# Kernel tuning notes

Measured on AMD Instinct MI355X. Metric: run time of the kernel, lower is better.

## Reference

```python
import jax, jax.numpy as jnp
import numpy as np

N = 50000
E = 400000
F_IN = 5
H = 8
C1, C2, C3 = 64, 32, 16
NEG_SLOPE = 0.2


def setup_inputs() -> dict:
    key = jax.random.key(0)
    ks = jax.random.split(key, 16)
    s = 0.1  # small init scale
    return {
        "x": jax.random.normal(ks[0], (N, F_IN), jnp.float32),
        "edge_index": jax.random.randint(ks[1], (2, E), 0, N, jnp.int64),
        "edge_weight": jax.random.uniform(ks[2], (E,), jnp.float32),
        "W1": jax.random.normal(ks[3], (F_IN, H * C1), jnp.float32) * s,
        "a_src1": jax.random.normal(ks[4], (H, C1), jnp.float32) * s,
        "a_dst1": jax.random.normal(ks[5], (H, C1), jnp.float32) * s,
        "b1": jnp.zeros((H * C1,), jnp.float32),
        "W2": jax.random.normal(ks[6], (H * C1, H * C2), jnp.float32) * s,
        "a_src2": jax.random.normal(ks[7], (H, C2), jnp.float32) * s,
        "a_dst2": jax.random.normal(ks[8], (H, C2), jnp.float32) * s,
        "b2": jnp.zeros((H * C2,), jnp.float32),
        "Wg": jax.random.normal(ks[9], (H * C2, C3), jnp.float32) * s,
        "bg": jnp.zeros((C3,), jnp.float32),
        "Wfc": jax.random.normal(ks[10], (C3, 1), jnp.float32) * s,
        "bfc": jnp.zeros((1,), jnp.float32),
    }


def _gat_layer(x, W, a_src, a_dst, b, src, dst, n, heads, ch):
    # PyG GATConv (concat=True), eval mode (dropout off), self-loops already in src/dst.
    h = (x @ W).reshape(n, heads, ch)                      # (N, H, C)
    e_s = jnp.sum(h * a_src, axis=-1)                      # (N, H)
    e_d = jnp.sum(h * a_dst, axis=-1)                      # (N, H)
    e = jax.nn.leaky_relu(e_s[src] + e_d[dst], NEG_SLOPE)  # (Etot, H)
    m = jax.ops.segment_max(e, dst, num_segments=n)
    m = jnp.where(jnp.isfinite(m), m, 0.0)                 # guard empty segments
    ex = jnp.exp(e - m[dst])
    den = jax.ops.segment_sum(ex, dst, num_segments=n)
    alpha = ex / (den[dst] + 1e-16)                        # softmax over in-edges
    out = jax.ops.segment_sum(h[src] * alpha[..., None], dst, num_segments=n)
    return out.reshape(n, heads * ch) + b


def _gcn_layer(x, W, b, src, dst, w_full, n):
    # PyG GCNConv with gcn_norm: D^{-1/2} A_hat D^{-1/2}, self-loop weight 1.
    deg = jax.ops.segment_sum(w_full, dst, num_segments=n)
    dinv = jnp.where(deg > 0, jax.lax.rsqrt(deg), 0.0)
    norm = dinv[src] * w_full * dinv[dst]                  # (Etot,)
    h = x @ W                                              # (N, C3)
    out = jax.ops.segment_sum(h[src] * norm[:, None], dst, num_segments=n)
    return out + b


def reference(x, edge_index, edge_weight, W1, a_src1, a_dst1, b1,
              W2, a_src2, a_dst2, b2, Wg, bg, Wfc, bfc):
    n = x.shape[0]
    loops = jnp.arange(n, dtype=edge_index.dtype)
    src = jnp.concatenate([edge_index[0], loops])
    dst = jnp.concatenate([edge_index[1], loops])
    w_full = jnp.concatenate([edge_weight, jnp.ones((n,), edge_weight.dtype)])

    h = _gat_layer(x, W1, a_src1, a_dst1, b1, src, dst, n, H, C1)
    h = jax.nn.elu(h)
    h = _gat_layer(h, W2, a_src2, a_dst2, b2, src, dst, n, H, C2)
    h = jax.nn.elu(h)
    h = _gcn_layer(h, Wg, bg, src, dst, w_full, n)
    h = jax.nn.elu(h)
    out = jax.nn.sigmoid(h @ Wfc + bfc)                    # (N, 1)
    return out
```

## Files before the change

### kernel.cpp

```cpp
#include <hip/hip_runtime.h>
#include <hip/hip_bf16.h>
#include <float.h>
#include <math.h>

#define N_NODES 50000
#define N_EDGES 400000
#define ETOT    (N_EDGES + N_NODES)
#define F_IN    5
#define HEADS   8
#define C1      64
#define C2      32
#define C3      16
#define HC1     (HEADS * C1)
#define HC2     (HEADS * C2)
#define NEG_SLOPE 0.2f
#define NCHUNK  ((N_NODES + 255) / 256)
#define NH8     (N_NODES * HEADS)
#define MPAD    (((N_NODES + 63) / 64) * 64)
#define GCOLS   (HC2 + 16)
#define PACKBLK ((GCOLS * HC1) / 256)
#define SCATBLK ((ETOT + 255) / 256)
#define ES1BLK  ((NH8 + 255) / 256)

typedef short bf16x8 __attribute__((ext_vector_type(8)));
typedef float f32x4  __attribute__((ext_vector_type(4)));
typedef unsigned short ushort_t;
typedef unsigned short ushort8_t __attribute__((ext_vector_type(8)));

__device__ __forceinline__ float eluf(float x) {
    return x > 0.f ? x : (expf(x) - 1.f);
}
__device__ __forceinline__ float bf2f(unsigned short u) {
    union { unsigned int i; float f; } v; v.i = ((unsigned int)u) << 16; return v.f;
}
__device__ __forceinline__ unsigned short f2bf(float f) {
    __hip_bfloat16 b = __float2bfloat16(f);
    return *(unsigned short*)&b;
}
__device__ __forceinline__ float softnum(float es, float ed) {
    float v = es + ed;
    v = v > 0.f ? v : NEG_SLOPE * v;
    return expf(v);
}

__global__ void k_deg(const int* __restrict__ ei, const float* __restrict__ ew,
                      int* degi, float* degf) {
    int i = blockIdx.x * blockDim.x + threadIdx.x;
    if (i >= ETOT) return;
    int d   = (i < N_EDGES) ? ei[N_EDGES + i] : (i - N_EDGES);
    float w = (i < N_EDGES) ? ew[i] : 1.f;
    atomicAdd(&degi[d], 1);
    atomicAdd(&degf[d], w);
}

__global__ void k_scan_a(const int* __restrict__ deg, int* __restrict__ part) {
    __shared__ int lds[256];
    int t = threadIdx.x;
    int i = blockIdx.x * 256 + t;
    lds[t] = (i < N_NODES) ? deg[i] : 0;
    __syncthreads();
    for (int off = 128; off >= 1; off >>= 1) {
        if (t < off) lds[t] += lds[t + off];
        __syncthreads();
    }
    if (t == 0) part[blockIdx.x] = lds[0];
}

__global__ void k_scan_b(int* part) {
    __shared__ int lds[256];
    int t = threadIdx.x;
    int v = (t < NCHUNK) ? part[t] : 0;
    lds[t] = v;
    __syncthreads();
    for (int off = 1; off < 256; off <<= 1) {
        int x = (t >= off) ? lds[t - off] : 0;
        __syncthreads();
        lds[t] += x;
        __syncthreads();
    }
    if (t < NCHUNK) part[t] = lds[t] - v;
}

__global__ void k_scan_c(const int* __restrict__ deg, const int* __restrict__ part,
                         int* __restrict__ offs) {
    __shared__ int lds[256];
    int t = threadIdx.x;
    int i = blockIdx.x * 256 + t;
    int v = (i < N_NODES) ? deg[i] : 0;
    lds[t] = v;
    __syncthreads();
    for (int off = 1; off < 256; off <<= 1) {
        int x = (t >= off) ? lds[t - off] : 0;
        __syncthreads();
        lds[t] += x;
        __syncthreads();
    }
    int excl = part[blockIdx.x] + lds[t] - v;
    if (i < N_NODES) offs[i] = excl;
    if (i == N_NODES - 1) offs[N_NODES] = excl + v;
}

__global__ void k_prep(const float* __restrict__ W2,
                       const float* __restrict__ a_src2, const float* __restrict__ a_dst2,
                       ushort_t* __restrict__ W2X,
                       const float* __restrict__ W1,
                       const float* __restrict__ a_src1, const float* __restrict__ a_dst1,
                       float* __restrict__ as1f, float* __restrict__ ad1f) {
    if (blockIdx.x < PACKBLK) {
        int idx = blockIdx.x * 256 + threadIdx.x;
        int c = idx >> 9;
        int k = idx & 511;
        float v;
        if (c < HC2) {
            v = W2[(size_t)k * HC2 + c];
        } else {
            int h = (c - HC2) & 7;
            const float* av = (c < HC2 + 8) ? a_src2 : a_dst2;
            v = 0.f;
#pragma unroll 8
            for (int j = 0; j < C2; j++)
                v += W2[(size_t)k * HC2 + h * C2 + j] * av[h * C2 + j];
        }
        W2X[idx] = f2bf(v);
    } else {
        int idx = threadIdx.x;
        if (idx >= HEADS * F_IN) return;
        int h = idx / F_IN, f = idx % F_IN;
        float s = 0.f, d = 0.f;
        for (int c = 0; c < C1; c++) {
            float w = W1[f * HC1 + h * C1 + c];
            s += w * a_src1[h * C1 + c];
            d += w * a_dst1[h * C1 + c];
        }
        as1f[idx] = s;
        ad1f[idx] = d;
    }
}

__global__ void k_scatter_es1(const int* __restrict__ ei, const int* __restrict__ offs,
                              int* cursor, int2* __restrict__ csr,
                              const float* __restrict__ x,
                              const float* __restrict__ as1f, const float* __restrict__ ad1f,
                              float* __restrict__ es, float* __restrict__ ed) {
    if (blockIdx.x < SCATBLK) {
        int i = blockIdx.x * 256 + threadIdx.x;
        if (i >= ETOT) return;
        int s, d;
        if (i < N_EDGES) { s = ei[i]; d = ei[N_EDGES + i]; }
        else             { s = d = i - N_EDGES; }
        int pos = offs[d] + atomicAdd(&cursor[d], 1);
        csr[pos] = make_int2(s, i);
    } else {
        int g = (blockIdx.x - SCATBLK) * 256 + threadIdx.x;
        if (g >= NH8) return;
        int n = g >> 3, h = g & 7;
        float vs = 0.f, vd = 0.f;
#pragma unroll
        for (int f = 0; f < F_IN; f++) {
            float xv = x[n * F_IN + f];
            vs += xv * as1f[h * F_IN + f];
            vd += xv * ad1f[h * F_IN + f];
        }
        es[g] = vs;
        ed[g] = vd;
    }
}

__global__ void k_agg_x(const float* __restrict__ x,
                        const float* __restrict__ es1, const float* __restrict__ ed1,
                        const int* __restrict__ offs, const int2* __restrict__ csr,
                        float* __restrict__ aggx) {
    int g = blockIdx.x * blockDim.x + threadIdx.x;
    if (g >= NH8) return;
    int d = g >> 3, h = g & 7;
    float edv = ed1[g];
    int k0 = offs[d], k1 = offs[d + 1];
    float a0 = 0.f, a1 = 0.f, a2 = 0.f, a3 = 0.f, a4 = 0.f, exsum = 0.f;
    int k = k0;
    if (k + 1 < k1) {
        int2 c0 = csr[k], c1 = csr[k + 1];
        for (; k + 3 < k1; k += 2) {
            int2 n0 = csr[k + 2], n1 = csr[k + 3];
            float x0 = softnum(es1[c0.x * HEADS + h], edv);
            float x1 = softnum(es1[c1.x * HEADS + h], edv);
            const float* xp0 = x + c0.x * F_IN;
            const float* xp1 = x + c1.x * F_IN;
            a0 += x0 * xp0[0] + x1 * xp1[0];
            a1 += x0 * xp0[1] + x1 * xp1[1];
            a2 += x0 * xp0[2] + x1 * xp1[2];
            a3 += x0 * xp0[3] + x1 * xp1[3];
            a4 += x0 * xp0[4] + x1 * xp1[4];
            exsum += x0 + x1;
            c0 = n0; c1 = n1;
        }
        {
            float x0 = softnum(es1[c0.x * HEADS + h], edv);
            float x1 = softnum(es1[c1.x * HEADS + h], edv);
            const float* xp0 = x + c0.x * F_IN;
            const float* xp1 = x + c1.x * F_IN;
            a0 += x0 * xp0[0] + x1 * xp1[0];
            a1 += x0 * xp0[1] + x1 * xp1[1];
            a2 += x0 * xp0[2] + x1 * xp1[2];
            a3 += x0 * xp0[3] + x1 * xp1[3];
            a4 += x0 * xp0[4] + x1 * xp1[4];
            exsum += x0 + x1;
            k += 2;
        }
    }
    if (k < k1) {
        int2 c0 = csr[k];
        float x0 = softnum(es1[c0.x * HEADS + h], edv);
        const float* xp0 = x + c0.x * F_IN;
        a0 += x0 * xp0[0];
        a1 += x0 * xp0[1];
        a2 += x0 * xp0[2];
        a3 += x0 * xp0[3];
        a4 += x0 * xp0[4];
        exsum += x0;
    }
    float inv = 1.f / (exsum + 1e-16f);
    aggx[0 * NH8 + g] = a0 * inv;
    aggx[1 * NH8 + g] = a1 * inv;
    aggx[2 * NH8 + g] = a2 * inv;
    aggx[3 * NH8 + g] = a3 * inv;
    aggx[4 * NH8 + g] = a4 * inv;
}

__global__ __launch_bounds__(256) void k_expand(const float* __restrict__ aggx,
                                                const float* __restrict__ W1,
                                                const float* __restrict__ b1,
                                                ushort_t* __restrict__ x2bf) {
    int wave = threadIdx.x >> 6;
    int j    = threadIdx.x & 63;
    int n    = blockIdx.x * 4 + wave;
    if (n >= N_NODES) return;
    int h = j >> 3;
    int g = n * HEADS + h;
    float av[F_IN];
#pragma unroll
    for (int f = 0; f < F_IN; f++) av[f] = aggx[f * NH8 + g];

    const float* w1p = W1 + j * 8;
    float4 s0 = *(const float4*)(b1 + j * 8);
    float4 s1 = *(const float4*)(b1 + j * 8 + 4);
#pragma unroll
    for (int f = 0; f < F_IN; f++) {
        float4 w0  = *(const float4*)(w1p + f * HC1);
        float4 w1v = *(const float4*)(w1p + f * HC1 + 4);
        s0.x += av[f] * w0.x;  s0.y += av[f] * w0.y;
        s0.z += av[f] * w0.z;  s0.w += av[f] * w0.w;
        s1.x += av[f] * w1v.x; s1.y += av[f] * w1v.y;
        s1.z += av[f] * w1v.z; s1.w += av[f] * w1v.w;
    }
    ushort8_t o;
    o[0] = f2bf(eluf(s0.x)); o[1] = f2bf(eluf(s0.y));
    o[2] = f2bf(eluf(s0.z)); o[3] = f2bf(eluf(s0.w));
    o[4] = f2bf(eluf(s1.x)); o[5] = f2bf(eluf(s1.y));
    o[6] = f2bf(eluf(s1.z)); o[7] = f2bf(eluf(s1.w));
    *(ushort8_t*)(x2bf + (size_t)n * HC1 + j * 8) = o;
}

__global__ __launch_bounds__(256, 3) void k_gemm_mfma(const short* __restrict__ A,
                                                      const short* __restrict__ W2X,
                                                      ushort_t* __restrict__ h2bf,
                                                      float* __restrict__ es2,
                                                      float* __restrict__ ed2) {
    __shared__ short Bs[GCOLS * 32];
    int t    = threadIdx.x;
    int wave = t >> 6;
    int lane = t & 63;
    int lo   = lane & 15;
    int quad = lane >> 4;
    int m0   = blockIdx.x * 64 + wave * 16;
    const short* ap = A + (size_t)(m0 + lo) * HC1 + quad * 8;

    f32x4 acc[17];
#pragma unroll
    for (int f = 0; f < 17; f++) acc[f] = (f32x4){0.f, 0.f, 0.f, 0.f};

    for (int idx = t; idx < GCOLS * 4; idx += 256) {
        int c = idx >> 2, q = idx & 3;
        int s = (q + c + (c >> 2)) & 3;
        *(bf16x8*)(Bs + c * 32 + s * 8) = *(const bf16x8*)(W2X + (size_t)c * HC1 + q * 8);
    }
    __syncthreads();

#pragma unroll 1
    for (int k0 = 0; k0 < HC1; k0 += 32) {
        int nk = k0 + 32;
        bf16x8 pre[5];
        if (nk < HC1) {
#pragma unroll
            for (int j = 0; j < 5; j++) {
                int idx = t + j * 256;
                if (idx < GCOLS * 4) {
                    int c = idx >> 2, q = idx & 3;
                    pre[j] = *(const bf16x8*)(W2X + (size_t)c * HC1 + nk + q * 8);
                }
            }
        }
        bf16x8 aF = *(const bf16x8*)(ap + k0);
#pragma unroll
        for (int f = 0; f < 17; f++) {
            int c = f * 16 + lo;
            int s = (quad + c + (c >> 2)) & 3;
            bf16x8 bF = *(const bf16x8*)(Bs + c * 32 + s * 8);
            acc[f] = __builtin_amdgcn_mfma_f32_16x16x32_bf16(aF, bF, acc[f], 0, 0, 0);
        }
        __syncthreads();
        if (nk < HC1) {
#pragma unroll
            for (int j = 0; j < 5; j++) {
                int idx = t + j * 256;
                if (idx < GCOLS * 4) {
                    int c = idx >> 2, q = idx & 3;
                    int s = (q + c + (c >> 2)) & 3;
                    *(bf16x8*)(Bs + c * 32 + s * 8) = pre[j];
                }
            }
            __syncthreads();
        }
    }

    int rowb = m0 + quad * 4;
#pragma unroll
    for (int f = 0; f < 16; f++) {
#pragma unroll
        for (int r = 0; r < 4; r++) {
            int row = rowb + r;
            if (row < N_NODES)
                h2bf[(size_t)row * HC2 + f * 16 + lo] = f2bf(acc[f][r]);
        }
    }
#pragma unroll
    for (int r = 0; r < 4; r++) {
        int row = rowb + r;
        if (row < N_NODES) {
            if (lo < 8) es2[row * HEADS + lo]       = acc[16][r];
            else        ed2[row * HEADS + (lo - 8)] = acc[16][r];
        }
    }
}

__global__ __launch_bounds__(256) void k_gat_agg2(const ushort_t* __restrict__ h2bf,
                                                  const float* __restrict__ es2,
                                                  const float* __restrict__ ed2,
                                                  const int* __restrict__ offs,
                                                  const int2* __restrict__ csr,
                                                  const float* __restrict__ b2,
                                                  ushort_t* __restrict__ x3bf) {
    int wave = threadIdx.x >> 6;
    int lane = threadIdx.x & 63;
    int d = blockIdx.x * 4 + wave;
    if (d >= N_NODES) return;
    int c4 = lane * 4;
    int h  = lane >> 3;
    float edv = ed2[d * HEADS + h];
    int k0 = offs[d], k1 = offs[d + 1];
    float acc0 = 0.f, acc1 = 0.f, acc2 = 0.f, acc3 = 0.f, exsum = 0.f;
    int k = k0;
    if (k + 1 < k1) {
        int2 e0 = csr[k], e1 = csr[k + 1];
        for (; k + 3 < k1; k += 2) {
            int2 n0 = csr[k + 2], n1 = csr[k + 3];
            float x0 = softnum(es2[e0.x * HEADS + h], edv);
            float x1 = softnum(es2[e1.x * HEADS + h], edv);
            ushort4 v0 = *(const ushort4*)(h2bf + (size_t)e0.x * HC2 + c4);
            ushort4 v1 = *(const ushort4*)(h2bf + (size_t)e1.x * HC2 + c4);
            acc0 += x0 * bf2f(v0.x) + x1 * bf2f(v1.x);
            acc1 += x0 * bf2f(v0.y) + x1 * bf2f(v1.y);
            acc2 += x0 * bf2f(v0.z) + x1 * bf2f(v1.z);
            acc3 += x0 * bf2f(v0.w) + x1 * bf2f(v1.w);
            exsum += x0 + x1;
            e0 = n0; e1 = n1;
        }
        {
            float x0 = softnum(es2[e0.x * HEADS + h], edv);
            float x1 = softnum(es2[e1.x * HEADS + h], edv);
            ushort4 v0 = *(const ushort4*)(h2bf + (size_t)e0.x * HC2 + c4);
            ushort4 v1 = *(const ushort4*)(h2bf + (size_t)e1.x * HC2 + c4);
            acc0 += x0 * bf2f(v0.x) + x1 * bf2f(v1.x);
            acc1 += x0 * bf2f(v0.y) + x1 * bf2f(v1.y);
            acc2 += x0 * bf2f(v0.z) + x1 * bf2f(v1.z);
            acc3 += x0 * bf2f(v0.w) + x1 * bf2f(v1.w);
            exsum += x0 + x1;
            k += 2;
        }
    }
    if (k < k1) {
        int2 e0 = csr[k];
        float x0 = softnum(es2[e0.x * HEADS + h], edv);
        ushort4 v0 = *(const ushort4*)(h2bf + (size_t)e0.x * HC2 + c4);
        acc0 += x0 * bf2f(v0.x);
        acc1 += x0 * bf2f(v0.y);
        acc2 += x0 * bf2f(v0.z);
        acc3 += x0 * bf2f(v0.w);
        exsum += x0;
    }
    float inv = 1.f / (exsum + 1e-16f);
    float4 bias = *(const float4*)(b2 + c4);
    ushort4 o;
    o.x = f2bf(eluf(acc0 * inv + bias.x));
    o.y = f2bf(eluf(acc1 * inv + bias.y));
    o.z = f2bf(eluf(acc2 * inv + bias.z));
    o.w = f2bf(eluf(acc3 * inv + bias.w));
    *(ushort4*)(x3bf + (size_t)d * HC2 + c4) = o;
}

__global__ __launch_bounds__(256) void k_hg(const ushort_t* __restrict__ x3bf,
                                            const float* __restrict__ Wg,
                                            float* __restrict__ hg) {
    __shared__ float xs[16 * HC2];
    int n0 = blockIdx.x * 16;
    int t  = threadIdx.x;
    for (int q = t; q < 16 * HC2 / 4; q += 256) {
        int r  = q >> 6;
        int cc = (q & 63) * 4;
        int n  = n0 + r;
        ushort4 v = make_ushort4(0, 0, 0, 0);
        if (n < N_NODES) v = *(const ushort4*)(x3bf + (size_t)n * HC2 + cc);
        xs[r * HC2 + cc + 0] = bf2f(v.x);
        xs[r * HC2 + cc + 1] = bf2f(v.y);
        xs[r * HC2 + cc + 2] = bf2f(v.z);
        xs[r * HC2 + cc + 3] = bf2f(v.w);
    }
    __syncthreads();
    int r = t >> 4, c = t & 15;
    float acc = 0.f;
#pragma unroll 4
    for (int k = 0; k < HC2; k++) acc += xs[r * HC2 + k] * Wg[k * C3 + c];
    int n = n0 + r;
    if (n < N_NODES) hg[(size_t)n * C3 + c] = acc;
}

__global__ __launch_bounds__(256) void k_gcn_out(const float* __restrict__ hg,
                                                 const float* __restrict__ ew,
                                                 const float* __restrict__ degf,
                                                 const int* __restrict__ offs,
                                                 const int2* __restrict__ csr,
                                                 const float* __restrict__ bg,
                                                 const float* __restrict__ Wfc,
                                                 const float* __restrict__ bfc,
                                                 float* __restrict__ out) {
    int t = threadIdx.x;
    int r = t >> 4, c = t & 15;
    int d = blockIdx.x * 16 + r;
    float val = 0.f;
    if (d < N_NODES) {
        float dd = degf[d];
        float dinv_d = dd > 0.f ? rsqrtf(dd) : 0.f;
        int k0 = offs[d], k1 = offs[d + 1];
        float acc = 0.f;
        for (int k = k0; k < k1; k++) {
            int2 se = csr[k];
            float w = (se.y < N_EDGES) ? ew[se.y] : 1.f;
            float ds_ = degf[se.x];
            float dinv_s = ds_ > 0.f ? rsqrtf(ds_) : 0.f;
            acc += hg[(size_t)se.x * C3 + c] * (dinv_s * w * dinv_d);
        }
        val = eluf(acc + bg[c]);
    }
    float z = val * Wfc[c];
#pragma unroll
    for (int off = 8; off >= 1; off >>= 1) z += __shfl_xor(z, off, 16);
    if (c == 0 && d < N_NODES) out[d] = 1.f / (1.f + expf(-(z + bfc[0])));
}

extern "C" void kernel_launch(void* const* d_in, const int* in_sizes, int n_in,
                              void* d_out, int out_size, void* d_ws, size_t ws_size,
                              hipStream_t stream) {
    const float* x       = (const float*)d_in[0];
    const int*   ei      = (const int*)  d_in[1];
    const float* ew      = (const float*)d_in[2];
    const float* W1      = (const float*)d_in[3];
    const float* a_src1  = (const float*)d_in[4];
    const float* a_dst1  = (const float*)d_in[5];
    const float* b1      = (const float*)d_in[6];
    const float* W2      = (const float*)d_in[7];
    const float* a_src2  = (const float*)d_in[8];
    const float* a_dst2  = (const float*)d_in[9];
    const float* b2      = (const float*)d_in[10];
    const float* Wg      = (const float*)d_in[11];
    const float* bg      = (const float*)d_in[12];
    const float* Wfc     = (const float*)d_in[13];
    const float* bfc     = (const float*)d_in[14];
    float* out = (float*)d_out;

    char* w = (char*)d_ws;
    size_t off = 0;
    auto alloc = [&](size_t bytes) -> void* {
        void* p = w + off;
        off = (off + bytes + 255) & ~(size_t)255;
        return p;
    };
    ushort_t* x2bf = (ushort_t*)alloc((size_t)MPAD * HC1 * 2);
    ushort_t* W2X  = (ushort_t*)alloc((size_t)GCOLS * HC1 * 2);
    ushort_t* h2bf = (ushort_t*)alloc((size_t)N_NODES * HC2 * 2);
    ushort_t* x3bf = (ushort_t*)alloc((size_t)N_NODES * HC2 * 2);
    float* hg     = (float*)alloc((size_t)N_NODES * C3 * 4);
    float* aggx   = (float*)alloc((size_t)F_IN * NH8 * 4);
    float* es1    = (float*)alloc((size_t)NH8 * 4);
    float* ed1    = (float*)alloc((size_t)NH8 * 4);
    float* es2    = (float*)alloc((size_t)NH8 * 4);
    float* ed2    = (float*)alloc((size_t)NH8 * 4);
    float* as1f   = (float*)alloc((size_t)HEADS * F_IN * 4);
    float* ad1f   = (float*)alloc((size_t)HEADS * F_IN * 4);
    float* degf   = (float*)alloc((size_t)N_NODES * 4);
    int*   degi   = (int*)  alloc((size_t)N_NODES * 4);
    int*   cursor = (int*)  alloc((size_t)N_NODES * 4);
    char*  zero_end = w + off;
    int*   offs   = (int*)  alloc((size_t)(N_NODES + 1) * 4);
    int*   part   = (int*)  alloc(256 * 4);
    int2*  csr    = (int2*) alloc((size_t)ETOT * 8);

    const int T = 256;
    hipMemsetAsync(degf, 0, (size_t)(zero_end - (char*)degf), stream);
    k_deg<<<dim3((ETOT + T - 1) / T), dim3(T), 0, stream>>>(ei, ew, degi, degf);
    k_scan_a<<<dim3(NCHUNK), dim3(256), 0, stream>>>(degi, part);
    k_scan_b<<<dim3(1), dim3(256), 0, stream>>>(part);
    k_scan_c<<<dim3(NCHUNK), dim3(256), 0, stream>>>(degi, part, offs);
    k_prep<<<dim3(PACKBLK + 1), dim3(256), 0, stream>>>(
        W2, a_src2, a_dst2, W2X, W1, a_src1, a_dst1, as1f, ad1f);
    k_scatter_es1<<<dim3(SCATBLK + ES1BLK), dim3(256), 0, stream>>>(
        ei, offs, cursor, csr, x, as1f, ad1f, es1, ed1);

    k_agg_x<<<dim3((NH8 + T - 1) / T), dim3(T), 0, stream>>>(x, es1, ed1, offs, csr, aggx);
    k_expand<<<dim3((N_NODES + 3) / 4), dim3(256), 0, stream>>>(aggx, W1, b1, x2bf);

    k_gemm_mfma<<<dim3(MPAD / 64), dim3(256), 0, stream>>>(
        (const short*)x2bf, (const short*)W2X, h2bf, es2, ed2);
    k_gat_agg2<<<dim3((N_NODES + 3) / 4), dim3(256), 0, stream>>>(
        h2bf, es2, ed2, offs, csr, b2, x3bf);

    k_hg<<<dim3((N_NODES + 15) / 16), dim3(256), 0, stream>>>(x3bf, Wg, hg);
    k_gcn_out<<<dim3((N_NODES + 15) / 16), dim3(256), 0, stream>>>(
        hg, ew, degf, offs, csr, bg, Wfc, bfc, out);
}
```

Baseline: 328.3 us.

## Precompute GCN edge norms into CSR, pad x to 8 floats, vectorize hg

The second field of each CSR entry now holds the GCN normalization (dinv[s]*w*dinv[d]) instead of the original edge id. dinv is computed once per node in the scan kernel. This removes the edge-weight and degree gathers and rsqrt work from k_gcn_out, whose loop is also software-pipelined. x is padded to 8 floats per node so the layer-1 aggregation can use float4 loads, and k_hg reads a padded LDS row with float4. The cost is an extra padded copy of x and dinv gathers in the scatter kernel.

```diff
diff --git a/kernel.cpp b/kernel.cpp
--- a/kernel.cpp
+++ b/kernel.cpp
@@ -21,6 +21,8 @@
 #define PACKBLK ((GCOLS * HC1) / 256)
 #define SCATBLK ((ETOT + 255) / 256)
 #define ES1BLK  ((NH8 + 255) / 256)
+#define DEGBLK  SCATBLK
+#define XPBLK   ((N_NODES * 8 + 255) / 256)
 
 typedef short bf16x8 __attribute__((ext_vector_type(8)));
 typedef float f32x4  __attribute__((ext_vector_type(4)));
@@ -44,13 +46,21 @@
 }
 
 __global__ void k_deg(const int* __restrict__ ei, const float* __restrict__ ew,
-                      int* degi, float* degf) {
-    int i = blockIdx.x * blockDim.x + threadIdx.x;
-    if (i >= ETOT) return;
-    int d   = (i < N_EDGES) ? ei[N_EDGES + i] : (i - N_EDGES);
-    float w = (i < N_EDGES) ? ew[i] : 1.f;
-    atomicAdd(&degi[d], 1);
-    atomicAdd(&degf[d], w);
+                      int* degi, float* degf,
+                      const float* __restrict__ x, float* __restrict__ xp8) {
+    if (blockIdx.x < DEGBLK) {
+        int i = blockIdx.x * blockDim.x + threadIdx.x;
+        if (i >= ETOT) return;
+        int d   = (i < N_EDGES) ? ei[N_EDGES + i] : (i - N_EDGES);
+        float w = (i < N_EDGES) ? ew[i] : 1.f;
+        atomicAdd(&degi[d], 1);
+        atomicAdd(&degf[d], w);
+    } else {
+        int g = (blockIdx.x - DEGBLK) * 256 + threadIdx.x;
+        if (g >= N_NODES * 8) return;
+        int n = g >> 3, f = g & 7;
+        xp8[g] = (f < F_IN) ? x[n * F_IN + f] : 0.f;
+    }
 }
 
 __global__ void k_scan_a(const int* __restrict__ deg, int* __restrict__ part) {
@@ -82,7 +92,8 @@
 }
 
 __global__ void k_scan_c(const int* __restrict__ deg, const int* __restrict__ part,
-                         int* __restrict__ offs) {
+                         int* __restrict__ offs,
+                         const float* __restrict__ degf, float* __restrict__ dinv) {
     __shared__ int lds[256];
     int t = threadIdx.x;
     int i = blockIdx.x * 256 + t;
@@ -96,7 +107,11 @@
         __syncthreads();
     }
     int excl = part[blockIdx.x] + lds[t] - v;
-    if (i < N_NODES) offs[i] = excl;
+    if (i < N_NODES) {
+        offs[i] = excl;
+        float dd = degf[i];
+        dinv[i] = dd > 0.f ? rsqrtf(dd) : 0.f;
+    }
     if (i == N_NODES - 1) offs[N_NODES] = excl + v;
 }
 
@@ -139,6 +154,7 @@
 
 __global__ void k_scatter_es1(const int* __restrict__ ei, const int* __restrict__ offs,
                               int* cursor, int2* __restrict__ csr,
+                              const float* __restrict__ ew, const float* __restrict__ dinv,
                               const float* __restrict__ x,
                               const float* __restrict__ as1f, const float* __restrict__ ad1f,
                               float* __restrict__ es, float* __restrict__ ed) {
@@ -146,10 +162,12 @@
         int i = blockIdx.x * 256 + threadIdx.x;
         if (i >= ETOT) return;
         int s, d;
-        if (i < N_EDGES) { s = ei[i]; d = ei[N_EDGES + i]; }
-        else             { s = d = i - N_EDGES; }
+        float w;
+        if (i < N_EDGES) { s = ei[i]; d = ei[N_EDGES + i]; w = ew[i]; }
+        else             { s = d = i - N_EDGES; w = 1.f; }
+        float nrm = dinv[s] * w * dinv[d];
         int pos = offs[d] + atomicAdd(&cursor[d], 1);
-        csr[pos] = make_int2(s, i);
+        csr[pos] = make_int2(s, __float_as_int(nrm));
     } else {
         int g = (blockIdx.x - SCATBLK) * 256 + threadIdx.x;
         if (g >= NH8) return;
@@ -166,7 +184,7 @@
     }
 }
 
-__global__ void k_agg_x(const float* __restrict__ x,
+__global__ void k_agg_x(const float* __restrict__ xp8,
                         const float* __restrict__ es1, const float* __restrict__ ed1,
                         const int* __restrict__ offs, const int2* __restrict__ csr,
                         float* __restrict__ aggx) {
@@ -183,26 +201,30 @@
             int2 n0 = csr[k + 2], n1 = csr[k + 3];
             float x0 = softnum(es1[c0.x * HEADS + h], edv);
             float x1 = softnum(es1[c1.x * HEADS + h], edv);
-            const float* xp0 = x + c0.x * F_IN;
-            const float* xp1 = x + c1.x * F_IN;
-            a0 += x0 * xp0[0] + x1 * xp1[0];
-            a1 += x0 * xp0[1] + x1 * xp1[1];
-            a2 += x0 * xp0[2] + x1 * xp1[2];
-            a3 += x0 * xp0[3] + x1 * xp1[3];
-            a4 += x0 * xp0[4] + x1 * xp1[4];
+            float4 A0 = *(const float4*)(xp8 + (size_t)c0.x * 8);
+            float  B0 = xp8[(size_t)c0.x * 8 + 4];
+            float4 A1 = *(const float4*)(xp8 + (size_t)c1.x * 8);
+            float  B1 = xp8[(size_t)c1.x * 8 + 4];
+            a0 += x0 * A0.x + x1 * A1.x;
+            a1 += x0 * A0.y + x1 * A1.y;
+            a2 += x0 * A0.z + x1 * A1.z;
+            a3 += x0 * A0.w + x1 * A1.w;
+            a4 += x0 * B0   + x1 * B1;
             exsum += x0 + x1;
             c0 = n0; c1 = n1;
         }
         {
             float x0 = softnum(es1[c0.x * HEADS + h], edv);
             float x1 = softnum(es1[c1.x * HEADS + h], edv);
-            const float* xp0 = x + c0.x * F_IN;
-            const float* xp1 = x + c1.x * F_IN;
-            a0 += x0 * xp0[0] + x1 * xp1[0];
-            a1 += x0 * xp0[1] + x1 * xp1[1];
-            a2 += x0 * xp0[2] + x1 * xp1[2];
-            a3 += x0 * xp0[3] + x1 * xp1[3];
-            a4 += x0 * xp0[4] + x1 * xp1[4];
+            float4 A0 = *(const float4*)(xp8 + (size_t)c0.x * 8);
+            float  B0 = xp8[(size_t)c0.x * 8 + 4];
+            float4 A1 = *(const float4*)(xp8 + (size_t)c1.x * 8);
+            float  B1 = xp8[(size_t)c1.x * 8 + 4];
+            a0 += x0 * A0.x + x1 * A1.x;
+            a1 += x0 * A0.y + x1 * A1.y;
+            a2 += x0 * A0.z + x1 * A1.z;
+            a3 += x0 * A0.w + x1 * A1.w;
+            a4 += x0 * B0   + x1 * B1;
             exsum += x0 + x1;
             k += 2;
         }
@@ -210,12 +232,13 @@
     if (k < k1) {
         int2 c0 = csr[k];
         float x0 = softnum(es1[c0.x * HEADS + h], edv);
-        const float* xp0 = x + c0.x * F_IN;
-        a0 += x0 * xp0[0];
-        a1 += x0 * xp0[1];
-        a2 += x0 * xp0[2];
-        a3 += x0 * xp0[3];
-        a4 += x0 * xp0[4];
+        float4 A0 = *(const float4*)(xp8 + (size_t)c0.x * 8);
+        float  B0 = xp8[(size_t)c0.x * 8 + 4];
+        a0 += x0 * A0.x;
+        a1 += x0 * A0.y;
+        a2 += x0 * A0.z;
+        a3 += x0 * A0.w;
+        a4 += x0 * B0;
         exsum += x0;
     }
     float inv = 1.f / (exsum + 1e-16f);
@@ -410,7 +433,7 @@
 __global__ __launch_bounds__(256) void k_hg(const ushort_t* __restrict__ x3bf,
                                             const float* __restrict__ Wg,
                                             float* __restrict__ hg) {
-    __shared__ float xs[16 * HC2];
+    __shared__ float xs[16 * 260];
     int n0 = blockIdx.x * 16;
     int t  = threadIdx.x;
     for (int q = t; q < 16 * HC2 / 4; q += 256) {
@@ -419,23 +442,28 @@
         int n  = n0 + r;
         ushort4 v = make_ushort4(0, 0, 0, 0);
         if (n < N_NODES) v = *(const ushort4*)(x3bf + (size_t)n * HC2 + cc);
-        xs[r * HC2 + cc + 0] = bf2f(v.x);
-        xs[r * HC2 + cc + 1] = bf2f(v.y);
-        xs[r * HC2 + cc + 2] = bf2f(v.z);
-        xs[r * HC2 + cc + 3] = bf2f(v.w);
+        xs[r * 260 + cc + 0] = bf2f(v.x);
+        xs[r * 260 + cc + 1] = bf2f(v.y);
+        xs[r * 260 + cc + 2] = bf2f(v.z);
+        xs[r * 260 + cc + 3] = bf2f(v.w);
     }
     __syncthreads();
     int r = t >> 4, c = t & 15;
+    const float* xr = xs + r * 260;
     float acc = 0.f;
-#pragma unroll 4
-    for (int k = 0; k < HC2; k++) acc += xs[r * HC2 + k] * Wg[k * C3 + c];
+#pragma unroll 8
+    for (int k = 0; k < HC2; k += 4) {
+        float4 v = *(const float4*)(xr + k);
+        acc += v.x * Wg[(k + 0) * C3 + c];
+        acc += v.y * Wg[(k + 1) * C3 + c];
+        acc += v.z * Wg[(k + 2) * C3 + c];
+        acc += v.w * Wg[(k + 3) * C3 + c];
+    }
     int n = n0 + r;
     if (n < N_NODES) hg[(size_t)n * C3 + c] = acc;
 }
 
 __global__ __launch_bounds__(256) void k_gcn_out(const float* __restrict__ hg,
-                                                 const float* __restrict__ ew,
-                                                 const float* __restrict__ degf,
                                                  const int* __restrict__ offs,
                                                  const int2* __restrict__ csr,
                                                  const float* __restrict__ bg,
@@ -447,16 +475,24 @@
     int d = blockIdx.x * 16 + r;
     float val = 0.f;
     if (d < N_NODES) {
-        float dd = degf[d];
-        float dinv_d = dd > 0.f ? rsqrtf(dd) : 0.f;
         int k0 = offs[d], k1 = offs[d + 1];
         float acc = 0.f;
-        for (int k = k0; k < k1; k++) {
-            int2 se = csr[k];
-            float w = (se.y < N_EDGES) ? ew[se.y] : 1.f;
-            float ds_ = degf[se.x];
-            float dinv_s = ds_ > 0.f ? rsqrtf(ds_) : 0.f;
-            acc += hg[(size_t)se.x * C3 + c] * (dinv_s * w * dinv_d);
+        int k = k0;
+        if (k + 1 < k1) {
+            int2 e0 = csr[k], e1 = csr[k + 1];
+            for (; k + 3 < k1; k += 2) {
+                int2 n0 = csr[k + 2], n1 = csr[k + 3];
+                acc += hg[(size_t)e0.x * C3 + c] * __int_as_float(e0.y);
+                acc += hg[(size_t)e1.x * C3 + c] * __int_as_float(e1.y);
+                e0 = n0; e1 = n1;
+            }
+            acc += hg[(size_t)e0.x * C3 + c] * __int_as_float(e0.y);
+            acc += hg[(size_t)e1.x * C3 + c] * __int_as_float(e1.y);
+            k += 2;
+        }
+        if (k < k1) {
+            int2 e0 = csr[k];
+            acc += hg[(size_t)e0.x * C3 + c] * __int_as_float(e0.y);
         }
         val = eluf(acc + bg[c]);
     }
@@ -512,19 +548,21 @@
     int*   offs   = (int*)  alloc((size_t)(N_NODES + 1) * 4);
     int*   part   = (int*)  alloc(256 * 4);
     int2*  csr    = (int2*) alloc((size_t)ETOT * 8);
+    float* dinv   = (float*)alloc((size_t)N_NODES * 4);
+    float* xp8    = (float*)alloc((size_t)N_NODES * 8 * 4);
 
     const int T = 256;
     hipMemsetAsync(degf, 0, (size_t)(zero_end - (char*)degf), stream);
-    k_deg<<<dim3((ETOT + T - 1) / T), dim3(T), 0, stream>>>(ei, ew, degi, degf);
+    k_deg<<<dim3(DEGBLK + XPBLK), dim3(T), 0, stream>>>(ei, ew, degi, degf, x, xp8);
     k_scan_a<<<dim3(NCHUNK), dim3(256), 0, stream>>>(degi, part);
     k_scan_b<<<dim3(1), dim3(256), 0, stream>>>(part);
-    k_scan_c<<<dim3(NCHUNK), dim3(256), 0, stream>>>(degi, part, offs);
+    k_scan_c<<<dim3(NCHUNK), dim3(256), 0, stream>>>(degi, part, offs, degf, dinv);
     k_prep<<<dim3(PACKBLK + 1), dim3(256), 0, stream>>>(
         W2, a_src2, a_dst2, W2X, W1, a_src1, a_dst1, as1f, ad1f);
     k_scatter_es1<<<dim3(SCATBLK + ES1BLK), dim3(256), 0, stream>>>(
-        ei, offs, cursor, csr, x, as1f, ad1f, es1, ed1);
-
-    k_agg_x<<<dim3((NH8 + T - 1) / T), dim3(T), 0, stream>>>(x, es1, ed1, offs, csr, aggx);
+        ei, offs, cursor, csr, ew, dinv, x, as1f, ad1f, es1, ed1);
+
+    k_agg_x<<<dim3((NH8 + T - 1) / T), dim3(T), 0, stream>>>(xp8, es1, ed1, offs, csr, aggx);
     k_expand<<<dim3((N_NODES + 3) / 4), dim3(256), 0, stream>>>(aggx, W1, b1, x2bf);
 
     k_gemm_mfma<<<dim3(MPAD / 64), dim3(256), 0, stream>>>(
@@ -534,5 +572,5 @@
 
     k_hg<<<dim3((N_NODES + 15) / 16), dim3(256), 0, stream>>>(x3bf, Wg, hg);
     k_gcn_out<<<dim3((N_NODES + 15) / 16), dim3(256), 0, stream>>>(
-        hg, ew, degf, offs, csr, bg, Wfc, bfc, out);
-}
+        hg, offs, csr, bg, Wfc, bfc, out);
+}
```

Result: faster. 311.3 us (-5.1%).
